# Performance work log

Hardware: AMD Instinct MI355X
Metric: run time of the kernel (lower is better)

Reference implementation:

```python
import jax, jax.numpy as jnp
import numpy as np

TAU = 2.0  # self.temperature
EPS = 1e-7

def setup_inputs() -> dict:
    key = jax.random.key(0)
    k1, k2, k3, k4, k5, k6 = jax.random.split(key, 6)
    B, S, H = 8, 4096, 512
    G, V, Dg = 2, 320, 128  # groups, codevectors per group, codevector_dim // G
    hidden_states = jax.random.normal(k1, (B, S, H), dtype=jnp.float32)
    mask_time_indices = jax.random.randint(k2, (B, S), 0, 2) > 0
    u = jax.random.uniform(k3, (B * S, G, V), dtype=jnp.float32, minval=1e-6, maxval=1.0 - 1e-6)
    gumbel_noise = -jnp.log(-jnp.log(u))  # standard Gumbel samples, as in F.gumbel_softmax
    W_proj = jax.random.normal(k4, (H, G * V), dtype=jnp.float32) * 0.02
    b_proj = jax.random.normal(k5, (G * V,), dtype=jnp.float32) * 0.02
    codevectors = jax.random.normal(k6, (G, V, Dg), dtype=jnp.float32)
    return {"hidden_states": hidden_states, "mask_time_indices": mask_time_indices,
            "gumbel_noise": gumbel_noise, "W_proj": W_proj, "b_proj": b_proj,
            "codevectors": codevectors}

def reference(hidden_states, mask_time_indices, gumbel_noise, W_proj, b_proj, codevectors):
    B, S, H = hidden_states.shape
    G, V, Dg = codevectors.shape
    N = B * S
    # weight projection: [B,S,H] -> [B,S,G*V] -> [N, G, V]
    logits = (jnp.einsum('bsh,hk->bsk', hidden_states, W_proj) + b_proj)
    logits = logits.reshape(N, G, V).astype(jnp.float32)
    # gumbel-softmax with hard=True (straight-through)
    y_soft = jax.nn.softmax((logits + gumbel_noise) / TAU, axis=-1)  # [N,G,V]
    idx = jnp.argmax(y_soft, axis=-1)                                 # [N,G]
    y_hard = jax.nn.one_hot(idx, V, dtype=y_soft.dtype)
    codevector_probs = y_hard + y_soft - jax.lax.stop_gradient(y_soft)
    # perplexity on the (noise-free) soft distribution, masked marginal
    soft_dist = jax.nn.softmax(logits, axis=-1)                       # [N,G,V]
    m = mask_time_indices.reshape(-1).astype(jnp.float32)             # [N]
    marginal = jnp.einsum('ngv,n->gv', soft_dist, m) / jnp.sum(m)
    perplexity = jnp.sum(jnp.exp(-jnp.sum(marginal * jnp.log(marginal + EPS), axis=-1)))
    # hard one-hot weighted sum over codebook == gather of selected codevector
    cv = jnp.einsum('ngv,gvd->ngd', codevector_probs, codevectors)    # [N,G,Dg]
    cv = cv.reshape(B, S, G * Dg)
    return cv, perplexity
```

## Files before the change

kernel.cpp:

```cpp
#include <hip/hip_runtime.h>
#include <hip/hip_bf16.h>
#include <math.h>

#define N_ROWS 32768
#define H      512
#define GV     640
#define V      320
#define DG     128
#define BM     64
#define NT     16

typedef __attribute__((ext_vector_type(4))) float f32x4;
typedef __attribute__((ext_vector_type(8))) short short8v;

static __device__ __forceinline__ short f2bf(float f) {
    unsigned int u = __float_as_uint(f);
    u += 0x7fffu + ((u >> 16) & 1u);
    return (short)(u >> 16);
}

static __device__ __forceinline__ void gload_lds16(const short* g, short* l) {
    __builtin_amdgcn_global_load_lds(
        (const __attribute__((address_space(1))) void*)g,
        (__attribute__((address_space(3))) void*)l, 16, 0, 0);
}

__global__ __launch_bounds__(256)
void pack_wa(const float* __restrict__ W, short* __restrict__ wp,
             const float* __restrict__ hidden, short* __restrict__ ap)
{
    if (blockIdx.x < 160) {
        int gid = blockIdx.x * 256 + threadIdx.x;
        int l   = gid & 63;
        int ct  = (gid >> 6) % 40;
        int t   = gid / (40 * 64);
        int row = t * 32 + 8 * (l >> 4);
        int col = ct * 16 + (l & 15);
        short8v pk;
        #pragma unroll
        for (int i = 0; i < 8; ++i)
            pk[i] = f2bf(W[(size_t)(row + i) * GV + col]);
        *(short8v*)(wp + (size_t)gid * 8) = pk;
    } else {
        int gid = (blockIdx.x - 160) * 256 + threadIdx.x;
        int l   = gid & 63;
        int t   = (gid >> 6) & 15;
        int rt  = gid >> 10;
        const float* src = hidden + (size_t)(rt * 16 + (l & 15)) * H + t * 32 + 8 * (l >> 4);
        float4 x0 = *(const float4*)src;
        float4 x1 = *(const float4*)(src + 4);
        short8v pk;
        pk[0] = f2bf(x0.x); pk[1] = f2bf(x0.y); pk[2] = f2bf(x0.z); pk[3] = f2bf(x0.w);
        pk[4] = f2bf(x1.x); pk[5] = f2bf(x1.y); pk[6] = f2bf(x1.z); pk[7] = f2bf(x1.w);
        *(short8v*)(ap + (size_t)gid * 8) = pk;
    }
}

__global__ __launch_bounds__(1024, 4)
void gumbel_vq_main(const short* apack,
                    const int*   __restrict__ mask,
                    const float* __restrict__ gumbel,
                    const short* __restrict__ wpack,
                    const float* __restrict__ bias,
                    const float* __restrict__ codevec,
                    float* out,
                    float* __restrict__ ws)
{
    __shared__ __align__(16) short sbuf[2][20480];
    float4 (*ex)[16]   = (float4 (*)[16])(&sbuf[0][0]);
    float*  ex2        = (float*)((char*)sbuf + 4096);
    float*  mg         = (float*)((char*)sbuf + 5120);
    int   (*rowtab)[2] = (int (*)[2])((char*)sbuf + 15360);

    const int tid = threadIdx.x;
    const int tn  = tid & 63;
    const int wid = tid >> 6;
    const int wm  = wid >> 2;
    const int wn  = wid & 3;
    const int q   = tn >> 4;
    const int cn  = tn & 15;
    const int row0 = blockIdx.x * BM;
    const int cbase = wn * 160 + cn;

    f32x4 acc[10];
    #pragma unroll
    for (int j = 0; j < 10; ++j) {
        float b = bias[cbase + j * 16];
        f32x4 c; c[0] = b; c[1] = b; c[2] = b; c[3] = b;
        acc[j] = c;
    }

    const short* ab = apack + ((size_t)(blockIdx.x * 4 + wm) * 1024 + tn) * 8;

    const bool xtra = (tid < 512);

    gload_lds16(wpack + (size_t)tid * 8,          &sbuf[0][(size_t)tid * 8]);
    gload_lds16(wpack + (size_t)(tid + 1024) * 8, &sbuf[0][(size_t)(tid + 1024) * 8]);
    if (xtra)
        gload_lds16(wpack + (size_t)(tid + 2048) * 8, &sbuf[0][(size_t)(tid + 2048) * 8]);
    short8v areg = *(const short8v*)ab;
    __syncthreads();

    #pragma unroll
    for (int t = 0; t < NT; ++t) {
        const int cur = t & 1;
        short8v anx;
        if (t + 1 < NT) {
            const short* wt = wpack + (size_t)(t + 1) * 20480;
            short* bd = &sbuf[cur ^ 1][0];
            gload_lds16(wt + (size_t)tid * 8,          bd + (size_t)tid * 8);
            gload_lds16(wt + (size_t)(tid + 1024) * 8, bd + (size_t)(tid + 1024) * 8);
            if (xtra)
                gload_lds16(wt + (size_t)(tid + 2048) * 8, bd + (size_t)(tid + 2048) * 8);
            anx = *(const short8v*)(ab + (size_t)(t + 1) * 512);
        }
        const short* bufc = &sbuf[cur][(size_t)(wn * 640 + tn) * 8];
        #pragma unroll
        for (int j = 0; j < 10; ++j) {
            short8v bf = *(const short8v*)(bufc + j * 512);
            acc[j] = __builtin_amdgcn_mfma_f32_16x16x32_bf16(areg, bf, acc[j], 0, 0, 0);
        }
        if (t + 1 < NT) areg = anx;
        __syncthreads();
    }

    const int rowbase = row0 + wm * 16;
    float g[4][10];
    #pragma unroll
    for (int r = 0; r < 4; ++r) {
        const float* gp = gumbel + (size_t)(rowbase + 4 * q + r) * GV + cbase;
        #pragma unroll
        for (int j = 0; j < 10; ++j) g[r][j] = gp[j * 16];
    }
    float mrow[4];
    #pragma unroll
    for (int r = 0; r < 4; ++r)
        mrow[r] = (mask[rowbase + 4 * q + r] != 0) ? 1.f : 0.f;

    float lm[4];
    #pragma unroll
    for (int r = 0; r < 4; ++r) {
        lm[r] = acc[0][r];
        #pragma unroll
        for (int j = 1; j < 10; ++j) lm[r] = fmaxf(lm[r], acc[j][r]);
    }
    #pragma unroll
    for (int d = 8; d >= 1; d >>= 1)
        #pragma unroll
        for (int r = 0; r < 4; ++r)
            lm[r] = fmaxf(lm[r], __shfl_xor(lm[r], d, 64));

    float zm[4]; int zi[4];
    #pragma unroll
    for (int r = 0; r < 4; ++r) {
        zm[r] = acc[0][r] + g[r][0]; zi[r] = cbase;
        #pragma unroll
        for (int j = 1; j < 10; ++j) {
            float zj = acc[j][r] + g[r][j];
            if (zj > zm[r]) { zm[r] = zj; zi[r] = cbase + 16 * j; }
        }
    }
    #pragma unroll
    for (int d = 8; d >= 1; d >>= 1) {
        #pragma unroll
        for (int r = 0; r < 4; ++r) {
            float oz = __shfl_xor(zm[r], d, 64); int oi = __shfl_xor(zi[r], d, 64);
            if (oz > zm[r] || (oz == zm[r] && oi < zi[r])) { zm[r] = oz; zi[r] = oi; }
        }
    }

    if (cn == 0) {
        #pragma unroll
        for (int r = 0; r < 4; ++r) {
            float4 e; e.x = zm[r]; e.y = __int_as_float(zi[r]); e.z = lm[r]; e.w = 0.f;
            ex[wid][4 * q + r] = e;
        }
    }
    __syncthreads();
    const int pw = wid ^ 1;
    #pragma unroll
    for (int r = 0; r < 4; ++r) {
        float4 e = ex[pw][4 * q + r];
        float pz = e.x; int pi = __float_as_int(e.y);
        if (pz > zm[r] || (pz == zm[r] && pi < zi[r])) { zm[r] = pz; zi[r] = pi; }
        lm[r] = fmaxf(lm[r], e.z);
    }

    float pm[4][10], ps[4];
    #pragma unroll
    for (int r = 0; r < 4; ++r) {
        ps[r] = 0.f;
        #pragma unroll
        for (int j = 0; j < 10; ++j) {
            float p = __expf(acc[j][r] - lm[r]);
            pm[r][j] = p; ps[r] += p;
        }
    }
    #pragma unroll
    for (int d = 8; d >= 1; d >>= 1)
        #pragma unroll
        for (int r = 0; r < 4; ++r)
            ps[r] += __shfl_xor(ps[r], d, 64);

    if (cn == 0) {
        #pragma unroll
        for (int r = 0; r < 4; ++r) ex2[wid * 16 + 4 * q + r] = ps[r];
    }
    __syncthreads();
    float inv[4];
    #pragma unroll
    for (int r = 0; r < 4; ++r)
        inv[r] = mrow[r] / (ps[r] + ex2[pw * 16 + 4 * q + r]);

    float part[10];
    #pragma unroll
    for (int j = 0; j < 10; ++j) {
        part[j] = pm[0][j] * inv[0] + pm[1][j] * inv[1] + pm[2][j] * inv[2] + pm[3][j] * inv[3];
        part[j] += __shfl_xor(part[j], 16, 64);
        part[j] += __shfl_xor(part[j], 32, 64);
    }
    if (q == 0) {
        #pragma unroll
        for (int j = 0; j < 10; ++j)
            mg[wm * GV + cbase + 16 * j] = part[j];
    }
    if ((wn == 0 || wn == 2) && cn == 0) {
        int grp = wn >> 1;
        #pragma unroll
        for (int r = 0; r < 4; ++r)
            rowtab[wm * 16 + 4 * q + r][grp] = zi[r] - grp * V;
    }
    __syncthreads();

    if (tid < GV)
        atomicAdd(&ws[tid], mg[tid] + mg[GV + tid] + mg[2 * GV + tid] + mg[3 * GV + tid]);
    if (wid == 0) {
        int mr = (mask[row0 + tn] != 0);
        unsigned long long b = __ballot(mr);
        if (tn == 0) atomicAdd(&ws[GV], (float)__popcll(b));
    }
    {
        const int row = tid >> 4;
        const int six = tid & 15;
        #pragma unroll
        for (int i = 0; i < 4; ++i) {
            int e4  = six + 16 * i;
            int grp = e4 >> 5;
            int off = e4 & 31;
            int idx = rowtab[row][grp];
            float4 vv = ((const float4*)(codevec + ((size_t)grp * V + idx) * DG))[off];
            ((float4*)(out + (size_t)(row0 + row) * (2 * DG)))[e4] = vv;
        }
    }
}

__global__ void gumbel_vq_finalize(const float* __restrict__ ws, float* __restrict__ out)
{
    __shared__ float red[GV];
    int t = threadIdx.x;
    float cnt = ws[GV];
    float p = ws[t] / cnt;
    red[t] = p * logf(p + 1e-7f);
    __syncthreads();
    if (t == 0) {
        float e0 = 0.f, e1 = 0.f;
        for (int i = 0; i < V; ++i)  e0 += red[i];
        for (int i = V; i < GV; ++i) e1 += red[i];
        out[(size_t)N_ROWS * 2 * DG] = expf(-e0) + expf(-e1);
    }
}

extern "C" void kernel_launch(void* const* d_in, const int* in_sizes, int n_in,
                              void* d_out, int out_size, void* d_ws, size_t ws_size,
                              hipStream_t stream)
{
    const float* hidden  = (const float*)d_in[0];
    const int*   mask    = (const int*)  d_in[1];
    const float* gumbel  = (const float*)d_in[2];
    const float* W       = (const float*)d_in[3];
    const float* bias    = (const float*)d_in[4];
    const float* codevec = (const float*)d_in[5];
    float* out = (float*)d_out;
    float* ws  = (float*)d_ws;
    short* wpack = (short*)((char*)d_ws + 4096);
    short* apack = (short*)d_out;

    hipMemsetAsync(d_ws, 0, (GV + 1) * sizeof(float), stream);
    pack_wa<<<8352, 256, 0, stream>>>(W, wpack, hidden, apack);
    gumbel_vq_main<<<N_ROWS / BM, 1024, 0, stream>>>(apack, mask, gumbel, wpack, bias, codevec, out, ws);
    gumbel_vq_finalize<<<1, GV, 0, stream>>>(ws, out);
}
```

Baseline: 90.96 us.

## Switch GEMM to 32x32x16 MFMA tiles with 512-thread blocks

Replaces the 16x16x32 bf16 MFMA with the 32x32x16 variant, repacking both the weight and activation layouts to match. Blocks shrink to 8 waves, each owning 32 rows by 160 columns with fewer, larger accumulators. The softmax, argmax and marginal epilogue is restructured into four row chunks, and the whole codevector gather is redone. The aim is higher MFMA throughput and fewer LDS B-fragment reads per FLOP, at the cost of more accumulator registers and extra block-wide barriers in the epilogue.

```diff
diff --git a/kernel.cpp b/kernel.cpp
--- a/kernel.cpp
+++ b/kernel.cpp
@@ -10,8 +10,8 @@
 #define BM     64
 #define NT     16
 
-typedef __attribute__((ext_vector_type(4))) float f32x4;
-typedef __attribute__((ext_vector_type(8))) short short8v;
+typedef __attribute__((ext_vector_type(16))) float f32x16;
+typedef __attribute__((ext_vector_type(8)))  short short8v;
 
 static __device__ __forceinline__ short f2bf(float f) {
     unsigned int u = __float_as_uint(f);
@@ -32,10 +32,10 @@
     if (blockIdx.x < 160) {
         int gid = blockIdx.x * 256 + threadIdx.x;
         int l   = gid & 63;
-        int ct  = (gid >> 6) % 40;
-        int t   = gid / (40 * 64);
-        int row = t * 32 + 8 * (l >> 4);
-        int col = ct * 16 + (l & 15);
+        int ct  = (gid >> 6) % 20;
+        int t2  = gid / (20 * 64);
+        int row = t2 * 16 + 8 * (l >> 5);
+        int col = ct * 32 + (l & 31);
         short8v pk;
         #pragma unroll
         for (int i = 0; i < 8; ++i)
@@ -43,10 +43,10 @@
         *(short8v*)(wp + (size_t)gid * 8) = pk;
     } else {
         int gid = (blockIdx.x - 160) * 256 + threadIdx.x;
-        int l   = gid & 63;
-        int t   = (gid >> 6) & 15;
-        int rt  = gid >> 10;
-        const float* src = hidden + (size_t)(rt * 16 + (l & 15)) * H + t * 32 + 8 * (l >> 4);
+        int l    = gid & 63;
+        int t2   = (gid >> 6) & 31;
+        int rt32 = gid >> 11;
+        const float* src = hidden + (size_t)(rt32 * 32 + (l & 31)) * H + t2 * 16 + 8 * (l >> 5);
         float4 x0 = *(const float4*)src;
         float4 x1 = *(const float4*)(src + 4);
         short8v pk;
@@ -56,7 +56,7 @@
     }
 }
 
-__global__ __launch_bounds__(1024, 4)
+__global__ __launch_bounds__(512, 4)
 void gumbel_vq_main(const short* apack,
                     const int*   __restrict__ mask,
                     const float* __restrict__ gumbel,
@@ -67,184 +67,185 @@
                     float* __restrict__ ws)
 {
     __shared__ __align__(16) short sbuf[2][20480];
-    float4 (*ex)[16]   = (float4 (*)[16])(&sbuf[0][0]);
+    float4 (*ex)[32]   = (float4 (*)[32])(&sbuf[0][0]);
     float*  ex2        = (float*)((char*)sbuf + 4096);
     float*  mg         = (float*)((char*)sbuf + 5120);
-    int   (*rowtab)[2] = (int (*)[2])((char*)sbuf + 15360);
+    int   (*rowtab)[2] = (int (*)[2])((char*)sbuf + 10240);
 
     const int tid = threadIdx.x;
     const int tn  = tid & 63;
     const int wid = tid >> 6;
     const int wm  = wid >> 2;
     const int wn  = wid & 3;
-    const int q   = tn >> 4;
-    const int cn  = tn & 15;
+    const int hi  = tn >> 5;
+    const int ln  = tn & 31;
     const int row0 = blockIdx.x * BM;
-    const int cbase = wn * 160 + cn;
-
-    f32x4 acc[10];
-    #pragma unroll
-    for (int j = 0; j < 10; ++j) {
-        float b = bias[cbase + j * 16];
-        f32x4 c; c[0] = b; c[1] = b; c[2] = b; c[3] = b;
+    const int colbase = wn * 160 + ln;
+
+    f32x16 acc[5];
+    #pragma unroll
+    for (int j = 0; j < 5; ++j) {
+        float b = bias[colbase + j * 32];
+        f32x16 c;
+        #pragma unroll
+        for (int r = 0; r < 16; ++r) c[r] = b;
         acc[j] = c;
     }
 
-    const short* ab = apack + ((size_t)(blockIdx.x * 4 + wm) * 1024 + tn) * 8;
-
-    const bool xtra = (tid < 512);
-
-    gload_lds16(wpack + (size_t)tid * 8,          &sbuf[0][(size_t)tid * 8]);
-    gload_lds16(wpack + (size_t)(tid + 1024) * 8, &sbuf[0][(size_t)(tid + 1024) * 8]);
-    if (xtra)
-        gload_lds16(wpack + (size_t)(tid + 2048) * 8, &sbuf[0][(size_t)(tid + 2048) * 8]);
-    short8v areg = *(const short8v*)ab;
+    const short* ab = apack + ((size_t)(blockIdx.x * 2 + wm) * 2048 + tn) * 8;
+
+    #pragma unroll
+    for (int k2 = 0; k2 < 5; ++k2)
+        gload_lds16(wpack + (size_t)(tid + k2 * 512) * 8, &sbuf[0][(size_t)(tid + k2 * 512) * 8]);
+    short8v a0reg = *(const short8v*)ab;
+    short8v a1reg = *(const short8v*)(ab + 512);
     __syncthreads();
 
     #pragma unroll
     for (int t = 0; t < NT; ++t) {
         const int cur = t & 1;
-        short8v anx;
+        short8v an0, an1;
         if (t + 1 < NT) {
             const short* wt = wpack + (size_t)(t + 1) * 20480;
             short* bd = &sbuf[cur ^ 1][0];
-            gload_lds16(wt + (size_t)tid * 8,          bd + (size_t)tid * 8);
-            gload_lds16(wt + (size_t)(tid + 1024) * 8, bd + (size_t)(tid + 1024) * 8);
-            if (xtra)
-                gload_lds16(wt + (size_t)(tid + 2048) * 8, bd + (size_t)(tid + 2048) * 8);
-            anx = *(const short8v*)(ab + (size_t)(t + 1) * 512);
-        }
-        const short* bufc = &sbuf[cur][(size_t)(wn * 640 + tn) * 8];
-        #pragma unroll
-        for (int j = 0; j < 10; ++j) {
-            short8v bf = *(const short8v*)(bufc + j * 512);
-            acc[j] = __builtin_amdgcn_mfma_f32_16x16x32_bf16(areg, bf, acc[j], 0, 0, 0);
-        }
-        if (t + 1 < NT) areg = anx;
+            #pragma unroll
+            for (int k2 = 0; k2 < 5; ++k2)
+                gload_lds16(wt + (size_t)(tid + k2 * 512) * 8, bd + (size_t)(tid + k2 * 512) * 8);
+            an0 = *(const short8v*)(ab + (size_t)(2 * t + 2) * 512);
+            an1 = *(const short8v*)(ab + (size_t)(2 * t + 3) * 512);
+        }
+        #pragma unroll
+        for (int j = 0; j < 5; ++j) {
+            short8v b0 = *(const short8v*)(&sbuf[cur][(size_t)((wn * 5 + j) * 64 + tn) * 8]);
+            acc[j] = __builtin_amdgcn_mfma_f32_32x32x16_bf16(a0reg, b0, acc[j], 0, 0, 0);
+            short8v b1 = *(const short8v*)(&sbuf[cur][(size_t)(((20 + wn * 5 + j)) * 64 + tn) * 8]);
+            acc[j] = __builtin_amdgcn_mfma_f32_32x32x16_bf16(a1reg, b1, acc[j], 0, 0, 0);
+        }
+        if (t + 1 < NT) { a0reg = an0; a1reg = an1; }
         __syncthreads();
     }
 
-    const int rowbase = row0 + wm * 16;
-    float g[4][10];
-    #pragma unroll
-    for (int r = 0; r < 4; ++r) {
-        const float* gp = gumbel + (size_t)(rowbase + 4 * q + r) * GV + cbase;
-        #pragma unroll
-        for (int j = 0; j < 10; ++j) g[r][j] = gp[j * 16];
-    }
-    float mrow[4];
-    #pragma unroll
-    for (int r = 0; r < 4; ++r)
-        mrow[r] = (mask[rowbase + 4 * q + r] != 0) ? 1.f : 0.f;
-
-    float lm[4];
-    #pragma unroll
-    for (int r = 0; r < 4; ++r) {
-        lm[r] = acc[0][r];
-        #pragma unroll
-        for (int j = 1; j < 10; ++j) lm[r] = fmaxf(lm[r], acc[j][r]);
-    }
-    #pragma unroll
-    for (int d = 8; d >= 1; d >>= 1)
-        #pragma unroll
-        for (int r = 0; r < 4; ++r)
-            lm[r] = fmaxf(lm[r], __shfl_xor(lm[r], d, 64));
-
-    float zm[4]; int zi[4];
-    #pragma unroll
-    for (int r = 0; r < 4; ++r) {
-        zm[r] = acc[0][r] + g[r][0]; zi[r] = cbase;
-        #pragma unroll
-        for (int j = 1; j < 10; ++j) {
-            float zj = acc[j][r] + g[r][j];
-            if (zj > zm[r]) { zm[r] = zj; zi[r] = cbase + 16 * j; }
-        }
-    }
-    #pragma unroll
-    for (int d = 8; d >= 1; d >>= 1) {
-        #pragma unroll
-        for (int r = 0; r < 4; ++r) {
-            float oz = __shfl_xor(zm[r], d, 64); int oi = __shfl_xor(zi[r], d, 64);
-            if (oz > zm[r] || (oz == zm[r] && oi < zi[r])) { zm[r] = oz; zi[r] = oi; }
-        }
-    }
-
-    if (cn == 0) {
-        #pragma unroll
-        for (int r = 0; r < 4; ++r) {
-            float4 e; e.x = zm[r]; e.y = __int_as_float(zi[r]); e.z = lm[r]; e.w = 0.f;
-            ex[wid][4 * q + r] = e;
-        }
+    const int rowbase = row0 + wm * 32;
+    const int pw = wid ^ 1;
+    float part[5];
+    #pragma unroll
+    for (int j = 0; j < 5; ++j) part[j] = 0.f;
+
+    #pragma unroll
+    for (int rc = 0; rc < 4; ++rc) {
+        float lm[4], zm[4]; int zi[4];
+        #pragma unroll
+        for (int rr = 0; rr < 4; ++rr) {
+            const int r = rc * 4 + rr;
+            float m_ = acc[0][r];
+            #pragma unroll
+            for (int j = 1; j < 5; ++j) m_ = fmaxf(m_, acc[j][r]);
+            lm[rr] = m_;
+        }
+        #pragma unroll
+        for (int rr = 0; rr < 4; ++rr) {
+            const int r = rc * 4 + rr;
+            const int R = 8 * rc + rr + 4 * hi;
+            const float* gp = gumbel + (size_t)(rowbase + R) * GV + colbase;
+            zm[rr] = acc[0][r] + gp[0]; zi[rr] = colbase;
+            #pragma unroll
+            for (int j = 1; j < 5; ++j) {
+                float zj = acc[j][r] + gp[32 * j];
+                if (zj > zm[rr]) { zm[rr] = zj; zi[rr] = colbase + 32 * j; }
+            }
+        }
+        #pragma unroll
+        for (int d = 16; d >= 1; d >>= 1) {
+            #pragma unroll
+            for (int rr = 0; rr < 4; ++rr) {
+                float oz = __shfl_xor(zm[rr], d, 64); int oi = __shfl_xor(zi[rr], d, 64);
+                if (oz > zm[rr] || (oz == zm[rr] && oi < zi[rr])) { zm[rr] = oz; zi[rr] = oi; }
+                lm[rr] = fmaxf(lm[rr], __shfl_xor(lm[rr], d, 64));
+            }
+        }
+        if (ln == 0) {
+            #pragma unroll
+            for (int rr = 0; rr < 4; ++rr) {
+                const int R = 8 * rc + rr + 4 * hi;
+                float4 e; e.x = zm[rr]; e.y = __int_as_float(zi[rr]); e.z = lm[rr]; e.w = 0.f;
+                ex[wid][R] = e;
+            }
+        }
+        __syncthreads();
+        #pragma unroll
+        for (int rr = 0; rr < 4; ++rr) {
+            const int R = 8 * rc + rr + 4 * hi;
+            float4 e = ex[pw][R];
+            float pz = e.x; int pi = __float_as_int(e.y);
+            if (pz > zm[rr] || (pz == zm[rr] && pi < zi[rr])) { zm[rr] = pz; zi[rr] = pi; }
+            lm[rr] = fmaxf(lm[rr], e.z);
+        }
+        float ps[4];
+        #pragma unroll
+        for (int rr = 0; rr < 4; ++rr) {
+            const int r = rc * 4 + rr;
+            float s = 0.f;
+            #pragma unroll
+            for (int j = 0; j < 5; ++j) s += __expf(acc[j][r] - lm[rr]);
+            ps[rr] = s;
+        }
+        #pragma unroll
+        for (int d = 16; d >= 1; d >>= 1)
+            #pragma unroll
+            for (int rr = 0; rr < 4; ++rr)
+                ps[rr] += __shfl_xor(ps[rr], d, 64);
+        if (ln == 0) {
+            #pragma unroll
+            for (int rr = 0; rr < 4; ++rr)
+                ex2[wid * 32 + (8 * rc + rr + 4 * hi)] = ps[rr];
+        }
+        __syncthreads();
+        float inv[4];
+        #pragma unroll
+        for (int rr = 0; rr < 4; ++rr) {
+            const int R = 8 * rc + rr + 4 * hi;
+            float mrow = (mask[rowbase + R] != 0) ? 1.f : 0.f;
+            inv[rr] = mrow / (ps[rr] + ex2[pw * 32 + R]);
+        }
+        #pragma unroll
+        for (int j = 0; j < 5; ++j) {
+            #pragma unroll
+            for (int rr = 0; rr < 4; ++rr) {
+                const int r = rc * 4 + rr;
+                part[j] += __expf(acc[j][r] - lm[rr]) * inv[rr];
+            }
+        }
+        if ((wn == 0 || wn == 2) && ln == 0) {
+            int grp = wn >> 1;
+            #pragma unroll
+            for (int rr = 0; rr < 4; ++rr)
+                rowtab[wm * 32 + (8 * rc + rr + 4 * hi)][grp] = zi[rr] - grp * V;
+        }
+    }
+
+    #pragma unroll
+    for (int j = 0; j < 5; ++j)
+        part[j] += __shfl_xor(part[j], 32, 64);
+    if (hi == 0) {
+        #pragma unroll
+        for (int j = 0; j < 5; ++j)
+            mg[wm * GV + colbase + 32 * j] = part[j];
     }
     __syncthreads();
-    const int pw = wid ^ 1;
-    #pragma unroll
-    for (int r = 0; r < 4; ++r) {
-        float4 e = ex[pw][4 * q + r];
-        float pz = e.x; int pi = __float_as_int(e.y);
-        if (pz > zm[r] || (pz == zm[r] && pi < zi[r])) { zm[r] = pz; zi[r] = pi; }
-        lm[r] = fmaxf(lm[r], e.z);
-    }
-
-    float pm[4][10], ps[4];
-    #pragma unroll
-    for (int r = 0; r < 4; ++r) {
-        ps[r] = 0.f;
-        #pragma unroll
-        for (int j = 0; j < 10; ++j) {
-            float p = __expf(acc[j][r] - lm[r]);
-            pm[r][j] = p; ps[r] += p;
-        }
-    }
-    #pragma unroll
-    for (int d = 8; d >= 1; d >>= 1)
-        #pragma unroll
-        for (int r = 0; r < 4; ++r)
-            ps[r] += __shfl_xor(ps[r], d, 64);
-
-    if (cn == 0) {
-        #pragma unroll
-        for (int r = 0; r < 4; ++r) ex2[wid * 16 + 4 * q + r] = ps[r];
-    }
-    __syncthreads();
-    float inv[4];
-    #pragma unroll
-    for (int r = 0; r < 4; ++r)
-        inv[r] = mrow[r] / (ps[r] + ex2[pw * 16 + 4 * q + r]);
-
-    float part[10];
-    #pragma unroll
-    for (int j = 0; j < 10; ++j) {
-        part[j] = pm[0][j] * inv[0] + pm[1][j] * inv[1] + pm[2][j] * inv[2] + pm[3][j] * inv[3];
-        part[j] += __shfl_xor(part[j], 16, 64);
-        part[j] += __shfl_xor(part[j], 32, 64);
-    }
-    if (q == 0) {
-        #pragma unroll
-        for (int j = 0; j < 10; ++j)
-            mg[wm * GV + cbase + 16 * j] = part[j];
-    }
-    if ((wn == 0 || wn == 2) && cn == 0) {
-        int grp = wn >> 1;
-        #pragma unroll
-        for (int r = 0; r < 4; ++r)
-            rowtab[wm * 16 + 4 * q + r][grp] = zi[r] - grp * V;
-    }
-    __syncthreads();
-
-    if (tid < GV)
-        atomicAdd(&ws[tid], mg[tid] + mg[GV + tid] + mg[2 * GV + tid] + mg[3 * GV + tid]);
+
+    for (int c = tid; c < GV; c += 512)
+        atomicAdd(&ws[c], mg[c] + mg[GV + c]);
     if (wid == 0) {
         int mr = (mask[row0 + tn] != 0);
         unsigned long long b = __ballot(mr);
         if (tn == 0) atomicAdd(&ws[GV], (float)__popcll(b));
     }
     {
-        const int row = tid >> 4;
-        const int six = tid & 15;
-        #pragma unroll
-        for (int i = 0; i < 4; ++i) {
-            int e4  = six + 16 * i;
+        const int row = tid >> 3;
+        const int six = tid & 7;
+        #pragma unroll
+        for (int i = 0; i < 8; ++i) {
+            int e4  = six + 8 * i;
             int grp = e4 >> 5;
             int off = e4 & 31;
             int idx = rowtab[row][grp];
@@ -287,6 +288,6 @@
 
     hipMemsetAsync(d_ws, 0, (GV + 1) * sizeof(float), stream);
     pack_wa<<<8352, 256, 0, stream>>>(W, wpack, hidden, apack);
-    gumbel_vq_main<<<N_ROWS / BM, 1024, 0, stream>>>(apack, mask, gumbel, wpack, bias, codevec, out, ws);
+    gumbel_vq_main<<<N_ROWS / BM, 512, 0, stream>>>(apack, mask, gumbel, wpack, bias, codevec, out, ws);
     gumbel_vq_finalize<<<1, GV, 0, stream>>>(ws, out);
 }
```

After: 132.9 us. 1.46x slower.
